# Performance work log

Measured on AMD Instinct MI355X. Metric: run time of the kernel, lower is better.

Reference implementation:

```python
import jax, jax.numpy as jnp
import numpy as np

H = 3072           # hidden_size
I = 8192           # intermediate_size
GS = 128           # quantization group size
B, S = 2, 2048


def dequant(qw, qz, scales, group_size=GS):
    """Group-wise int4 dequant: w = (q - zero) * scale.
    qw: [out, in] int8 nibbles in [0,16); qz: [out, in//g] int8; scales: [out, in//g] f32.
    """
    zp = jnp.repeat(qz.astype(jnp.float32), group_size, axis=1)
    sc = jnp.repeat(scales, group_size, axis=1)
    return (qw.astype(jnp.float32) - zp) * sc


def setup_inputs() -> dict:
    key = jax.random.key(0)
    ks = jax.random.split(key, 8)
    hidden_states = jax.random.normal(ks[0], (B, S, H), dtype=jnp.float32)
    # gate_up projection: [2*I, H], group-quantized along the input (H) dim
    gup_qw = jax.random.randint(ks[1], (2 * I, H), 0, 16, dtype=jnp.int8)
    gup_qz = jax.random.randint(ks[2], (2 * I, H // GS), 0, 16, dtype=jnp.int8)
    gup_scales = jax.random.uniform(ks[3], (2 * I, H // GS), dtype=jnp.float32, minval=0.005, maxval=0.02)
    # down projection: [H, I], group-quantized along the input (I) dim
    down_qw = jax.random.randint(ks[4], (H, I), 0, 16, dtype=jnp.int8)
    down_qz = jax.random.randint(ks[5], (H, I // GS), 0, 16, dtype=jnp.int8)
    down_scales = jax.random.uniform(ks[6], (H, I // GS), dtype=jnp.float32, minval=0.005, maxval=0.02)
    down_bias = jnp.zeros((H,), dtype=jnp.float32)
    return {
        "hidden_states": hidden_states,
        "gup_qw": gup_qw, "gup_qz": gup_qz, "gup_scales": gup_scales,
        "down_qw": down_qw, "down_qz": down_qz, "down_scales": down_scales,
        "down_bias": down_bias,
    }


def reference(hidden_states, gup_qw, gup_qz, gup_scales, down_qw, down_qz, down_scales, down_bias):
    W_gup = dequant(gup_qw, gup_qz, gup_scales)           # [2I, H]
    up_states = jnp.einsum('bsh,oh->bso', hidden_states, W_gup)  # [B,S,2I]
    gate, up = jnp.split(up_states, 2, axis=-1)
    act = jax.nn.silu(gate) * up                          # fused gate*act*up
    W_down = dequant(down_qw, down_qz, down_scales)       # [H, I]
    out = jnp.einsum('bsi,hi->bsh', act, W_down) + down_bias
    return out
```

## Files before the change

kernel.cpp:

```cpp
#include <hip/hip_runtime.h>


typedef float f32x4 __attribute__((ext_vector_type(4)));
typedef float f32x2 __attribute__((ext_vector_type(2)));
typedef int   i32x4 __attribute__((ext_vector_type(4)));

__device__ __forceinline__ void gload16(const void* g, void* l) {
  __builtin_amdgcn_global_load_lds(
      (const __attribute__((address_space(1))) void*)g,
      (__attribute__((address_space(3))) void*)l, 16, 0, 0);
}

__global__ __launch_bounds__(256) void quant_x(const float* __restrict__ x,
                                               signed char* __restrict__ Xq,
                                               float* __restrict__ Xs4) {
  int g    = blockIdx.x;
  int rq   = blockIdx.y;
  int w    = threadIdx.x >> 6;
  int lane = threadIdx.x & 63;
  int row  = rq * 4 + w;
  __shared__ float wmax[4];
  const float2 v = *(const float2*)(x + (size_t)row * 3072 + g * 128 + lane * 2);
  float m = fmaxf(fabsf(v.x), fabsf(v.y));
#pragma unroll
  for (int s = 1; s < 64; s <<= 1) m = fmaxf(m, __shfl_xor(m, s));
  if (lane == 0) wmax[w] = m;
  __syncthreads();
  float m4 = fmaxf(fmaxf(wmax[0], wmax[1]), fmaxf(wmax[2], wmax[3]));
  float inv = m4 > 0.f ? 127.f / m4 : 0.f;
  int qa = (int)rintf(v.x * inv);
  int qb = (int)rintf(v.y * inv);
  unsigned short pk = (unsigned short)((qa & 0xff) | ((qb & 0xff) << 8));
  *(unsigned short*)(Xq + (size_t)row * 3072 + g * 128 + lane * 2) = pk;
  if (threadIdx.x == 0) Xs4[g * 1024 + rq] = m4 * (1.f / 127.f);
}

template <int K>
__global__ __launch_bounds__(256) void requant_k(const int* __restrict__ qw,
                                                 const int* __restrict__ qz,
                                                 signed char* __restrict__ W) {
  constexpr int KG = K / 128;
  constexpr int perrow = K / 8;
  int idx = blockIdx.x * 256 + threadIdx.x;
  int row = idx / perrow;
  int c8  = idx - row * perrow;
  int k   = c8 << 3;
  int z   = qz[row * KG + (k >> 7)];
  const int4* q4 = (const int4*)(qw + (size_t)row * K + k);
  int4 qa = q4[0];
  int4 qb = q4[1];
  int b0 = ((qa.x - z) & 0xff) | (((qa.y - z) & 0xff) << 8) |
           (((qa.z - z) & 0xff) << 16) | (((qa.w - z) & 0xff) << 24);
  int b1 = ((qb.x - z) & 0xff) | (((qb.y - z) & 0xff) << 8) |
           (((qb.z - z) & 0xff) << 16) | (((qb.w - z) & 0xff) << 24);
  int2 o; o.x = b0; o.y = b1;
  *(int2*)(W + (size_t)row * K + k) = o;
}

__global__ __launch_bounds__(256) void transpose_sc(const float* __restrict__ in,
                                                    float* __restrict__ out,
                                                    int R, int G) {
  int idx = blockIdx.x * 256 + threadIdx.x;
  int r = idx / G;
  int g = idx - r * G;
  out[(size_t)g * R + r] = in[idx];
}


__global__ __launch_bounds__(256, 2) void gemm_gateup_i8(
    const signed char* __restrict__ Xq, const signed char* __restrict__ Wq,
    const float* __restrict__ Xs4,
    const float* __restrict__ GsT,
    signed char* __restrict__ act,
    float* __restrict__ As4) {
  const int K = 3072;
  const int bid = blockIdx.x;
  const int xcd = bid & 7;
  const int jb  = bid >> 3;
  const int n0  = ((xcd << 3) + (jb & 7)) * 128;
  const int m0  = (jb >> 3) * 128;
  __shared__ signed char lA[16384];
  __shared__ signed char lG[16384];
  __shared__ signed char lU[16384];
  __shared__ float rmax[2][128];
  __shared__ float rmax4[32];

  const int tid  = threadIdx.x;
  const int l    = tid & 63;
  const int quad = l >> 4;
  const int l16  = l & 15;
  const int wcI  = (tid >> 6) & 1;
  const int wr   = ((tid >> 6) >> 1) * 64;
  const int wc   = wcI * 64;

  f32x2 fg[4][4][2] = {};
  f32x2 fu[4][4][2] = {};

  int off[4];
#pragma unroll
  for (int jj = 0; jj < 4; ++jj) {
    int c   = tid + 256 * jj;
    int row = c >> 3;
    int log = (c & 7) ^ (row & 7);
    off[jj] = row * K + log * 16;
  }
  const signed char* baseA = Xq + (size_t)m0 * K;
  const signed char* baseG = Wq + (size_t)n0 * K;
  const signed char* baseU = Wq + (size_t)(8192 + n0) * K;

  int aoff[2][4], boff[2][4];
#pragma unroll
  for (int h = 0; h < 2; ++h) {
    int slot = h * 4 + quad;
#pragma unroll
    for (int i = 0; i < 4; ++i) {
      int ra = wr + i * 16 + l16;
      aoff[h][i] = ra * 128 + ((slot ^ (ra & 7)) * 16);
      int rb = wc + i * 16 + l16;
      boff[h][i] = rb * 128 + ((slot ^ (rb & 7)) * 16);
    }
  }
  const int qbase = (m0 >> 2) + (wr >> 2) + quad;

  for (int g = 0; g < 24; ++g) {
    const int kk = g << 7;
#pragma unroll
    for (int jj = 0; jj < 4; ++jj) {
      gload16(baseA + off[jj] + kk, lA + (tid + 256 * jj) * 16);
      gload16(baseG + off[jj] + kk, lG + (tid + 256 * jj) * 16);
      gload16(baseU + off[jj] + kk, lU + (tid + 256 * jj) * 16);
    }
    float sxq[4], sg[4], su[4];
#pragma unroll
    for (int i = 0; i < 4; ++i) sxq[i] = Xs4[g * 1024 + qbase + i * 4];
#pragma unroll
    for (int jj = 0; jj < 4; ++jj) {
      sg[jj] = GsT[g * 16384 + n0 + wc + jj * 16 + l16];
      su[jj] = GsT[g * 16384 + 8192 + n0 + wc + jj * 16 + l16];
    }
    __syncthreads();

    i32x4 a[4][2];
#pragma unroll
    for (int i = 0; i < 4; ++i) {
      a[i][0] = *(const i32x4*)(lA + aoff[0][i]);
      a[i][1] = *(const i32x4*)(lA + aoff[1][i]);
    }
#pragma unroll
    for (int jj = 0; jj < 4; ++jj) {
      i32x4 bg0 = *(const i32x4*)(lG + boff[0][jj]);
      i32x4 bg1 = *(const i32x4*)(lG + boff[1][jj]);
      i32x4 bu0 = *(const i32x4*)(lU + boff[0][jj]);
      i32x4 bu1 = *(const i32x4*)(lU + boff[1][jj]);
#pragma unroll
      for (int i = 0; i < 4; ++i) {
        i32x4 zero = {0, 0, 0, 0};
        i32x4 ig = __builtin_amdgcn_mfma_i32_16x16x64_i8(a[i][0], bg0, zero, 0, 0, 0);
        ig = __builtin_amdgcn_mfma_i32_16x16x64_i8(a[i][1], bg1, ig, 0, 0, 0);
        i32x4 iu = __builtin_amdgcn_mfma_i32_16x16x64_i8(a[i][0], bu0, zero, 0, 0, 0);
        iu = __builtin_amdgcn_mfma_i32_16x16x64_i8(a[i][1], bu1, iu, 0, 0, 0);
        float pgs = sxq[i] * sg[jj];
        float pus = sxq[i] * su[jj];
        f32x2 pg2 = {pgs, pgs};
        f32x2 pu2 = {pus, pus};
        f32x2 g01 = {(float)ig[0], (float)ig[1]};
        f32x2 g23 = {(float)ig[2], (float)ig[3]};
        f32x2 u01 = {(float)iu[0], (float)iu[1]};
        f32x2 u23 = {(float)iu[2], (float)iu[3]};
        fg[i][jj][0] = __builtin_elementwise_fma(g01, pg2, fg[i][jj][0]);
        fg[i][jj][1] = __builtin_elementwise_fma(g23, pg2, fg[i][jj][1]);
        fu[i][jj][0] = __builtin_elementwise_fma(u01, pu2, fu[i][jj][0]);
        fu[i][jj][1] = __builtin_elementwise_fma(u23, pu2, fu[i][jj][1]);
      }
    }
    __syncthreads();
  }

  float av[4][4][4];
#pragma unroll
  for (int i = 0; i < 4; ++i)
#pragma unroll
    for (int jj = 0; jj < 4; ++jj)
#pragma unroll
      for (int r = 0; r < 4; ++r) {
        float gv = fg[i][jj][r >> 1][r & 1];
        float uv = fu[i][jj][r >> 1][r & 1];
        av[i][jj][r] = (gv / (1.f + __expf(-gv))) * uv;
      }

#pragma unroll
  for (int i = 0; i < 4; ++i)
#pragma unroll
    for (int r = 0; r < 4; ++r) {
      float m = 0.f;
#pragma unroll
      for (int jj = 0; jj < 4; ++jj) m = fmaxf(m, fabsf(av[i][jj][r]));
      m = fmaxf(m, __shfl_xor(m, 1));
      m = fmaxf(m, __shfl_xor(m, 2));
      m = fmaxf(m, __shfl_xor(m, 4));
      m = fmaxf(m, __shfl_xor(m, 8));
      if (l16 == 0) rmax[wcI][wr + i * 16 + quad * 4 + r] = m;
    }
  __syncthreads();
  if (tid < 32) {
    float m = 0.f;
#pragma unroll
    for (int k = 0; k < 4; ++k)
      m = fmaxf(m, fmaxf(rmax[0][tid * 4 + k], rmax[1][tid * 4 + k]));
    rmax4[tid] = m;
    As4[(n0 >> 7) * 1024 + (m0 >> 2) + tid] = m * (1.f / 127.f);
  }
  __syncthreads();

#pragma unroll
  for (int i = 0; i < 4; ++i) {
    float mx = rmax4[(wr >> 2) + i * 4 + quad];
    float inv = mx > 0.f ? 127.f / mx : 0.f;
#pragma unroll
    for (int r = 0; r < 4; ++r) {
      int mrow = wr + i * 16 + quad * 4 + r;
#pragma unroll
      for (int jj = 0; jj < 4; ++jj) {
        int q = (int)rintf(av[i][jj][r] * inv);
        lA[mrow * 128 + wc + jj * 16 + l16] = (signed char)q;
      }
    }
  }
  __syncthreads();

#pragma unroll
  for (int t = 0; t < 4; ++t) {
    int c = tid + 256 * t;
    int row = c >> 3;
    int col = (c & 7) * 16;
    *(int4*)(act + (size_t)(m0 + row) * 8192 + n0 + col) = *(const int4*)(lA + row * 128 + col);
  }
}

__global__ __launch_bounds__(256, 2) void gemm_down_i8(
    const signed char* __restrict__ Aq, const signed char* __restrict__ Wq,
    const float* __restrict__ As4,
    const float* __restrict__ DsT,
    const float* __restrict__ bias,
    float* __restrict__ out) {
  const int K = 8192;
  const int bid = blockIdx.x;
  const int xcd = bid & 7;
  const int jb  = bid >> 3;
  const int jn  = jb % 12;
  const int jm  = jb / 12;
  const int n0  = (12 * (xcd & 1) + jn) * 128;
  const int m0  = (8 * (xcd >> 1) + jm) * 128;
  __shared__ signed char lA[16384];
  __shared__ signed char lB[16384];

  const int tid  = threadIdx.x;
  const int l    = tid & 63;
  const int quad = l >> 4;
  const int l16  = l & 15;
  const int wr   = ((tid >> 6) >> 1) * 64;
  const int wc   = ((tid >> 6) & 1) * 64;

  f32x2 fc[4][4][2] = {};

  int off[4];
#pragma unroll
  for (int jj = 0; jj < 4; ++jj) {
    int c   = tid + 256 * jj;
    int row = c >> 3;
    int log = (c & 7) ^ (row & 7);
    off[jj] = row * K + log * 16;
  }
  const signed char* baseA = Aq + (size_t)m0 * K;
  const signed char* baseB = Wq + (size_t)n0 * K;

  int aoff[2][4], boff[2][4];
#pragma unroll
  for (int h = 0; h < 2; ++h) {
    int slot = h * 4 + quad;
#pragma unroll
    for (int i = 0; i < 4; ++i) {
      int ra = wr + i * 16 + l16;
      aoff[h][i] = ra * 128 + ((slot ^ (ra & 7)) * 16);
      int rb = wc + i * 16 + l16;
      boff[h][i] = rb * 128 + ((slot ^ (rb & 7)) * 16);
    }
  }
  const int qbase = (m0 >> 2) + (wr >> 2) + quad;

  for (int g = 0; g < 64; ++g) {
    const int kk = g << 7;
#pragma unroll
    for (int jj = 0; jj < 4; ++jj) {
      gload16(baseA + off[jj] + kk, lA + (tid + 256 * jj) * 16);
      gload16(baseB + off[jj] + kk, lB + (tid + 256 * jj) * 16);
    }
    float sxq[4], sn[4];
#pragma unroll
    for (int i = 0; i < 4; ++i) sxq[i] = As4[g * 1024 + qbase + i * 4];
#pragma unroll
    for (int jj = 0; jj < 4; ++jj)
      sn[jj] = DsT[g * 3072 + n0 + wc + jj * 16 + l16];
    __syncthreads();

    i32x4 a[4][2];
#pragma unroll
    for (int i = 0; i < 4; ++i) {
      a[i][0] = *(const i32x4*)(lA + aoff[0][i]);
      a[i][1] = *(const i32x4*)(lA + aoff[1][i]);
    }
#pragma unroll
    for (int jj = 0; jj < 4; ++jj) {
      i32x4 b0 = *(const i32x4*)(lB + boff[0][jj]);
      i32x4 b1 = *(const i32x4*)(lB + boff[1][jj]);
#pragma unroll
      for (int i = 0; i < 4; ++i) {
        i32x4 zero = {0, 0, 0, 0};
        i32x4 ic = __builtin_amdgcn_mfma_i32_16x16x64_i8(a[i][0], b0, zero, 0, 0, 0);
        ic = __builtin_amdgcn_mfma_i32_16x16x64_i8(a[i][1], b1, ic, 0, 0, 0);
        float ps = sxq[i] * sn[jj];
        f32x2 p2 = {ps, ps};
        f32x2 c01 = {(float)ic[0], (float)ic[1]};
        f32x2 c23 = {(float)ic[2], (float)ic[3]};
        fc[i][jj][0] = __builtin_elementwise_fma(c01, p2, fc[i][jj][0]);
        fc[i][jj][1] = __builtin_elementwise_fma(c23, p2, fc[i][jj][1]);
      }
    }
    __syncthreads();
  }

  float bj[4];
#pragma unroll
  for (int jj = 0; jj < 4; ++jj) bj[jj] = bias[n0 + wc + jj * 16 + l16];

#pragma unroll
  for (int i = 0; i < 4; ++i)
#pragma unroll
    for (int jj = 0; jj < 4; ++jj)
#pragma unroll
      for (int r = 0; r < 4; ++r) {
        int m = m0 + wr + i * 16 + quad * 4 + r;
        int n = n0 + wc + jj * 16 + l16;
        out[(size_t)m * 3072 + n] = fc[i][jj][r >> 1][r & 1] + bj[jj];
      }
}

extern "C" void kernel_launch(void* const* d_in, const int* in_sizes, int n_in,
                              void* d_out, int out_size, void* d_ws, size_t ws_size,
                              hipStream_t stream) {
  const float* x        = (const float*)d_in[0];
  const int*   gup_qw   = (const int*)d_in[1];
  const int*   gup_qz   = (const int*)d_in[2];
  const float* gup_sc   = (const float*)d_in[3];
  const int*   down_qw  = (const int*)d_in[4];
  const int*   down_qz  = (const int*)d_in[5];
  const float* down_sc  = (const float*)d_in[6];
  const float* down_b   = (const float*)d_in[7];
  float* out = (float*)d_out;

  char* ws = (char*)d_ws;
  signed char* Xq    = (signed char*)(ws);
  signed char* Wgupq = (signed char*)(ws + 12582912);
  signed char* Wdnq  = (signed char*)(ws + 62914560);
  signed char* Actq  = (signed char*)(ws + 88080384);
  float* Xs4 = (float*)(ws + 121634816);
  float* GsT = (float*)(ws + 121733120);
  float* DsT = (float*)(ws + 123305984);
  float* As4 = (float*)(ws + 124092416);

  quant_x<<<dim3(24, 1024), 256, 0, stream>>>(x, Xq, Xs4);
  requant_k<3072><<<24576, 256, 0, stream>>>(gup_qw, gup_qz, Wgupq);
  requant_k<8192><<<12288, 256, 0, stream>>>(down_qw, down_qz, Wdnq);
  transpose_sc<<<1536, 256, 0, stream>>>(gup_sc, GsT, 16384, 24);
  transpose_sc<<<768, 256, 0, stream>>>(down_sc, DsT, 3072, 64);
  gemm_gateup_i8<<<2048, 256, 0, stream>>>(Xq, Wgupq, Xs4, GsT, Actq, As4);
  gemm_down_i8<<<768, 256, 0, stream>>>(Actq, Wdnq, As4, DsT, down_b, out);
}
```

Measured before the change: 799.0 us.

## Double-buffer LDS tiles in both int8 GEMMs and widen gate-up block to 512 threads

Both GEMMs now prefetch the next K-tile into a second LDS buffer while the MFMAs run on the current one. This replaces the load-then-sync-then-compute pattern with a single waitcnt+barrier per iteration, and wave priority is raised during the MFMA section. The gate-up kernel also moves to 512 threads (8 waves, each covering a 64x32 sub-tile) to cut per-thread accumulators and add waves. The cost is more LDS: 96KB for gate-up, which limits blocks per CU and may reduce occupancy.

```diff
diff --git a/kernel.cpp b/kernel.cpp
--- a/kernel.cpp
+++ b/kernel.cpp
@@ -67,7 +67,7 @@
 }
 
 
-__global__ __launch_bounds__(256, 2) void gemm_gateup_i8(
+__global__ __launch_bounds__(512, 2) void gemm_gateup_i8(
     const signed char* __restrict__ Xq, const signed char* __restrict__ Wq,
     const float* __restrict__ Xs4,
     const float* __restrict__ GsT,
@@ -79,36 +79,34 @@
   const int jb  = bid >> 3;
   const int n0  = ((xcd << 3) + (jb & 7)) * 128;
   const int m0  = (jb >> 3) * 128;
-  __shared__ signed char lA[16384];
-  __shared__ signed char lG[16384];
-  __shared__ signed char lU[16384];
-  __shared__ float rmax[2][128];
+  __shared__ __align__(16) signed char smem[98304];
+  __shared__ float rmax[4][128];
   __shared__ float rmax4[32];
 
   const int tid  = threadIdx.x;
   const int l    = tid & 63;
   const int quad = l >> 4;
   const int l16  = l & 15;
-  const int wcI  = (tid >> 6) & 1;
-  const int wr   = ((tid >> 6) >> 1) * 64;
-  const int wc   = wcI * 64;
-
-  f32x2 fg[4][4][2] = {};
-  f32x2 fu[4][4][2] = {};
-
-  int off[4];
-#pragma unroll
-  for (int jj = 0; jj < 4; ++jj) {
-    int c   = tid + 256 * jj;
+  const int w    = tid >> 6;
+  const int wr   = (w >> 2) * 64;
+  const int wc   = (w & 3) * 32;
+
+  f32x2 fg[4][2][2] = {};
+  f32x2 fu[4][2][2] = {};
+
+  int off[2];
+#pragma unroll
+  for (int t = 0; t < 2; ++t) {
+    int c   = tid + 512 * t;
     int row = c >> 3;
     int log = (c & 7) ^ (row & 7);
-    off[jj] = row * K + log * 16;
+    off[t] = row * K + log * 16;
   }
   const signed char* baseA = Xq + (size_t)m0 * K;
   const signed char* baseG = Wq + (size_t)n0 * K;
   const signed char* baseU = Wq + (size_t)(8192 + n0) * K;
 
-  int aoff[2][4], boff[2][4];
+  int aoff[2][4], boff[2][2];
 #pragma unroll
   for (int h = 0; h < 2; ++h) {
     int slot = h * 4 + quad;
@@ -116,42 +114,66 @@
     for (int i = 0; i < 4; ++i) {
       int ra = wr + i * 16 + l16;
       aoff[h][i] = ra * 128 + ((slot ^ (ra & 7)) * 16);
-      int rb = wc + i * 16 + l16;
-      boff[h][i] = rb * 128 + ((slot ^ (rb & 7)) * 16);
+    }
+#pragma unroll
+    for (int jj = 0; jj < 2; ++jj) {
+      int rb = wc + jj * 16 + l16;
+      boff[h][jj] = rb * 128 + ((slot ^ (rb & 7)) * 16);
     }
   }
   const int qbase = (m0 >> 2) + (wr >> 2) + quad;
 
+#pragma unroll
+  for (int t = 0; t < 2; ++t) {
+    gload16(baseA + off[t], smem + (tid + 512 * t) * 16);
+    gload16(baseG + off[t], smem + 16384 + (tid + 512 * t) * 16);
+    gload16(baseU + off[t], smem + 32768 + (tid + 512 * t) * 16);
+  }
+
+  int cur = 0;
   for (int g = 0; g < 24; ++g) {
-    const int kk = g << 7;
-#pragma unroll
-    for (int jj = 0; jj < 4; ++jj) {
-      gload16(baseA + off[jj] + kk, lA + (tid + 256 * jj) * 16);
-      gload16(baseG + off[jj] + kk, lG + (tid + 256 * jj) * 16);
-      gload16(baseU + off[jj] + kk, lU + (tid + 256 * jj) * 16);
-    }
-    float sxq[4], sg[4], su[4];
+    asm volatile("s_waitcnt vmcnt(0)" ::: "memory");
+    __builtin_amdgcn_s_barrier();
+    __builtin_amdgcn_sched_barrier(0);
+
+    float sxq[4], sg[2], su[2];
 #pragma unroll
     for (int i = 0; i < 4; ++i) sxq[i] = Xs4[g * 1024 + qbase + i * 4];
 #pragma unroll
-    for (int jj = 0; jj < 4; ++jj) {
+    for (int jj = 0; jj < 2; ++jj) {
       sg[jj] = GsT[g * 16384 + n0 + wc + jj * 16 + l16];
       su[jj] = GsT[g * 16384 + 8192 + n0 + wc + jj * 16 + l16];
     }
-    __syncthreads();
+    __builtin_amdgcn_sched_barrier(0);
+
+    if (g < 23) {
+      const int s1 = (cur ^ 1) * 49152;
+      const int kk = (g + 1) << 7;
+#pragma unroll
+      for (int t = 0; t < 2; ++t) {
+        gload16(baseA + off[t] + kk, smem + s1 + (tid + 512 * t) * 16);
+        gload16(baseG + off[t] + kk, smem + s1 + 16384 + (tid + 512 * t) * 16);
+        gload16(baseU + off[t] + kk, smem + s1 + 32768 + (tid + 512 * t) * 16);
+      }
+    }
+
+    const signed char* A0 = smem + cur * 49152;
+    const signed char* G0 = A0 + 16384;
+    const signed char* U0 = A0 + 32768;
 
     i32x4 a[4][2];
 #pragma unroll
     for (int i = 0; i < 4; ++i) {
-      a[i][0] = *(const i32x4*)(lA + aoff[0][i]);
-      a[i][1] = *(const i32x4*)(lA + aoff[1][i]);
-    }
-#pragma unroll
-    for (int jj = 0; jj < 4; ++jj) {
-      i32x4 bg0 = *(const i32x4*)(lG + boff[0][jj]);
-      i32x4 bg1 = *(const i32x4*)(lG + boff[1][jj]);
-      i32x4 bu0 = *(const i32x4*)(lU + boff[0][jj]);
-      i32x4 bu1 = *(const i32x4*)(lU + boff[1][jj]);
+      a[i][0] = *(const i32x4*)(A0 + aoff[0][i]);
+      a[i][1] = *(const i32x4*)(A0 + aoff[1][i]);
+    }
+    __builtin_amdgcn_s_setprio(1);
+#pragma unroll
+    for (int jj = 0; jj < 2; ++jj) {
+      i32x4 bg0 = *(const i32x4*)(G0 + boff[0][jj]);
+      i32x4 bg1 = *(const i32x4*)(G0 + boff[1][jj]);
+      i32x4 bu0 = *(const i32x4*)(U0 + boff[0][jj]);
+      i32x4 bu1 = *(const i32x4*)(U0 + boff[1][jj]);
 #pragma unroll
       for (int i = 0; i < 4; ++i) {
         i32x4 zero = {0, 0, 0, 0};
@@ -173,14 +195,15 @@
         fu[i][jj][1] = __builtin_elementwise_fma(u23, pu2, fu[i][jj][1]);
       }
     }
-    __syncthreads();
-  }
-
-  float av[4][4][4];
+    __builtin_amdgcn_s_setprio(0);
+    cur ^= 1;
+  }
+
+  float av[4][2][4];
 #pragma unroll
   for (int i = 0; i < 4; ++i)
 #pragma unroll
-    for (int jj = 0; jj < 4; ++jj)
+    for (int jj = 0; jj < 2; ++jj)
 #pragma unroll
       for (int r = 0; r < 4; ++r) {
         float gv = fg[i][jj][r >> 1][r & 1];
@@ -192,21 +215,20 @@
   for (int i = 0; i < 4; ++i)
 #pragma unroll
     for (int r = 0; r < 4; ++r) {
-      float m = 0.f;
-#pragma unroll
-      for (int jj = 0; jj < 4; ++jj) m = fmaxf(m, fabsf(av[i][jj][r]));
+      float m = fmaxf(fabsf(av[i][0][r]), fabsf(av[i][1][r]));
       m = fmaxf(m, __shfl_xor(m, 1));
       m = fmaxf(m, __shfl_xor(m, 2));
       m = fmaxf(m, __shfl_xor(m, 4));
       m = fmaxf(m, __shfl_xor(m, 8));
-      if (l16 == 0) rmax[wcI][wr + i * 16 + quad * 4 + r] = m;
+      if (l16 == 0) rmax[w & 3][wr + i * 16 + quad * 4 + r] = m;
     }
   __syncthreads();
   if (tid < 32) {
     float m = 0.f;
 #pragma unroll
-    for (int k = 0; k < 4; ++k)
-      m = fmaxf(m, fmaxf(rmax[0][tid * 4 + k], rmax[1][tid * 4 + k]));
+    for (int c = 0; c < 4; ++c)
+#pragma unroll
+      for (int k = 0; k < 4; ++k) m = fmaxf(m, rmax[c][tid * 4 + k]);
     rmax4[tid] = m;
     As4[(n0 >> 7) * 1024 + (m0 >> 2) + tid] = m * (1.f / 127.f);
   }
@@ -220,20 +242,20 @@
     for (int r = 0; r < 4; ++r) {
       int mrow = wr + i * 16 + quad * 4 + r;
 #pragma unroll
-      for (int jj = 0; jj < 4; ++jj) {
+      for (int jj = 0; jj < 2; ++jj) {
         int q = (int)rintf(av[i][jj][r] * inv);
-        lA[mrow * 128 + wc + jj * 16 + l16] = (signed char)q;
+        smem[mrow * 128 + wc + jj * 16 + l16] = (signed char)q;
       }
     }
   }
   __syncthreads();
 
 #pragma unroll
-  for (int t = 0; t < 4; ++t) {
-    int c = tid + 256 * t;
+  for (int t = 0; t < 2; ++t) {
+    int c = tid + 512 * t;
     int row = c >> 3;
     int col = (c & 7) * 16;
-    *(int4*)(act + (size_t)(m0 + row) * 8192 + n0 + col) = *(const int4*)(lA + row * 128 + col);
+    *(int4*)(act + (size_t)(m0 + row) * 8192 + n0 + col) = *(const int4*)(smem + row * 128 + col);
   }
 }
 
@@ -251,8 +273,7 @@
   const int jm  = jb / 12;
   const int n0  = (12 * (xcd & 1) + jn) * 128;
   const int m0  = (8 * (xcd >> 1) + jm) * 128;
-  __shared__ signed char lA[16384];
-  __shared__ signed char lB[16384];
+  __shared__ __align__(16) signed char smem[65536];
 
   const int tid  = threadIdx.x;
   const int l    = tid & 63;
@@ -288,31 +309,50 @@
   }
   const int qbase = (m0 >> 2) + (wr >> 2) + quad;
 
+#pragma unroll
+  for (int jj = 0; jj < 4; ++jj) {
+    gload16(baseA + off[jj], smem + (tid + 256 * jj) * 16);
+    gload16(baseB + off[jj], smem + 16384 + (tid + 256 * jj) * 16);
+  }
+
+  int cur = 0;
   for (int g = 0; g < 64; ++g) {
-    const int kk = g << 7;
-#pragma unroll
-    for (int jj = 0; jj < 4; ++jj) {
-      gload16(baseA + off[jj] + kk, lA + (tid + 256 * jj) * 16);
-      gload16(baseB + off[jj] + kk, lB + (tid + 256 * jj) * 16);
-    }
+    asm volatile("s_waitcnt vmcnt(0)" ::: "memory");
+    __builtin_amdgcn_s_barrier();
+    __builtin_amdgcn_sched_barrier(0);
+
     float sxq[4], sn[4];
 #pragma unroll
     for (int i = 0; i < 4; ++i) sxq[i] = As4[g * 1024 + qbase + i * 4];
 #pragma unroll
     for (int jj = 0; jj < 4; ++jj)
       sn[jj] = DsT[g * 3072 + n0 + wc + jj * 16 + l16];
-    __syncthreads();
+    __builtin_amdgcn_sched_barrier(0);
+
+    if (g < 63) {
+      const int s1 = (cur ^ 1) * 32768;
+      const int kk = (g + 1) << 7;
+#pragma unroll
+      for (int jj = 0; jj < 4; ++jj) {
+        gload16(baseA + off[jj] + kk, smem + s1 + (tid + 256 * jj) * 16);
+        gload16(baseB + off[jj] + kk, smem + s1 + 16384 + (tid + 256 * jj) * 16);
+      }
+    }
+
+    const signed char* A0 = smem + cur * 32768;
+    const signed char* B0 = A0 + 16384;
 
     i32x4 a[4][2];
 #pragma unroll
     for (int i = 0; i < 4; ++i) {
-      a[i][0] = *(const i32x4*)(lA + aoff[0][i]);
-      a[i][1] = *(const i32x4*)(lA + aoff[1][i]);
-    }
+      a[i][0] = *(const i32x4*)(A0 + aoff[0][i]);
+      a[i][1] = *(const i32x4*)(A0 + aoff[1][i]);
+    }
+    __builtin_amdgcn_s_setprio(1);
 #pragma unroll
     for (int jj = 0; jj < 4; ++jj) {
-      i32x4 b0 = *(const i32x4*)(lB + boff[0][jj]);
-      i32x4 b1 = *(const i32x4*)(lB + boff[1][jj]);
+      i32x4 b0 = *(const i32x4*)(B0 + boff[0][jj]);
+      i32x4 b1 = *(const i32x4*)(B0 + boff[1][jj]);
 #pragma unroll
       for (int i = 0; i < 4; ++i) {
         i32x4 zero = {0, 0, 0, 0};
@@ -326,7 +366,8 @@
         fc[i][jj][1] = __builtin_elementwise_fma(c23, p2, fc[i][jj][1]);
       }
     }
-    __syncthreads();
+    __builtin_amdgcn_s_setprio(0);
+    cur ^= 1;
   }
 
   float bj[4];
@@ -373,6 +414,6 @@
   requant_k<8192><<<12288, 256, 0, stream>>>(down_qw, down_qz, Wdnq);
   transpose_sc<<<1536, 256, 0, stream>>>(gup_sc, GsT, 16384, 24);
   transpose_sc<<<768, 256, 0, stream>>>(down_sc, DsT, 3072, 64);
-  gemm_gateup_i8<<<2048, 256, 0, stream>>>(Xq, Wgupq, Xs4, GsT, Actq, As4);
+  gemm_gateup_i8<<<2048, 512, 0, stream>>>(Xq, Wgupq, Xs4, GsT, Actq, As4);
   gemm_down_i8<<<768, 256, 0, stream>>>(Actq, Wdnq, As4, DsT, down_b, out);
 }
```

New measurement: 958.2 us. 19.9% more time.

## Use per-row scales for gate/up GEMM and accumulate int32 across K

Applied to the files above, without the earlier changes.

Activations are now quantized with one scale per 4-row block across the full hidden dimension instead of per 128-wide group. Gate/up weights are requantized to int8 with a single per-row scale that folds in the group scales, so the GEMM can accumulate in int32 over all of K and apply the scale once in the epilogue. This removes per-group int-to-float conversion and FMA work from the inner loop, along with the gate/up scale transpose kernel. It also adds s_setprio around the MFMA sections of both GEMMs. The trade-off is coarser quantization, which adds more rounding error to the weights and activations.

```diff
diff --git a/kernel.cpp b/kernel.cpp
--- a/kernel.cpp
+++ b/kernel.cpp
@@ -11,28 +11,68 @@
       (__attribute__((address_space(3))) void*)l, 16, 0, 0);
 }
 
-__global__ __launch_bounds__(256) void quant_x(const float* __restrict__ x,
-                                               signed char* __restrict__ Xq,
-                                               float* __restrict__ Xs4) {
-  int g    = blockIdx.x;
-  int rq   = blockIdx.y;
+__global__ __launch_bounds__(256) void quant_x_flat(const float* __restrict__ x,
+                                                    signed char* __restrict__ Xq,
+                                                    float* __restrict__ Xs) {
+  int rq   = blockIdx.x;
   int w    = threadIdx.x >> 6;
   int lane = threadIdx.x & 63;
-  int row  = rq * 4 + w;
+  size_t rowbase = ((size_t)rq * 4 + w) * 3072;
   __shared__ float wmax[4];
-  const float2 v = *(const float2*)(x + (size_t)row * 3072 + g * 128 + lane * 2);
-  float m = fmaxf(fabsf(v.x), fabsf(v.y));
+  float4 v[12];
+  float m = 0.f;
+#pragma unroll
+  for (int it = 0; it < 12; ++it) {
+    v[it] = *(const float4*)(x + rowbase + (lane + it * 64) * 4);
+    m = fmaxf(m, fmaxf(fmaxf(fabsf(v[it].x), fabsf(v[it].y)),
+                       fmaxf(fabsf(v[it].z), fabsf(v[it].w))));
+  }
 #pragma unroll
   for (int s = 1; s < 64; s <<= 1) m = fmaxf(m, __shfl_xor(m, s));
   if (lane == 0) wmax[w] = m;
   __syncthreads();
   float m4 = fmaxf(fmaxf(wmax[0], wmax[1]), fmaxf(wmax[2], wmax[3]));
   float inv = m4 > 0.f ? 127.f / m4 : 0.f;
-  int qa = (int)rintf(v.x * inv);
-  int qb = (int)rintf(v.y * inv);
-  unsigned short pk = (unsigned short)((qa & 0xff) | ((qb & 0xff) << 8));
-  *(unsigned short*)(Xq + (size_t)row * 3072 + g * 128 + lane * 2) = pk;
-  if (threadIdx.x == 0) Xs4[g * 1024 + rq] = m4 * (1.f / 127.f);
+#pragma unroll
+  for (int it = 0; it < 12; ++it) {
+    int a = (int)rintf(v[it].x * inv);
+    int b = (int)rintf(v[it].y * inv);
+    int c = (int)rintf(v[it].z * inv);
+    int d = (int)rintf(v[it].w * inv);
+    int pk = (a & 0xff) | ((b & 0xff) << 8) | ((c & 0xff) << 16) | ((d & 0xff) << 24);
+    *(int*)(Xq + rowbase + (lane + it * 64) * 4) = pk;
+  }
+  if (threadIdx.x == 0) Xs[rq] = m4 * (1.f / 127.f);
+}
+
+__global__ __launch_bounds__(256) void requant_gup_flat(const int* __restrict__ qw,
+                                                        const int* __restrict__ qz,
+                                                        const float* __restrict__ sc,
+                                                        signed char* __restrict__ W,
+                                                        float* __restrict__ Ws) {
+  int w    = threadIdx.x >> 6;
+  int lane = threadIdx.x & 63;
+  int r    = blockIdx.x * 4 + w;
+  float smax = (lane < 24) ? sc[r * 24 + lane] : 0.f;
+#pragma unroll
+  for (int s = 1; s < 64; s <<= 1) smax = fmaxf(smax, __shfl_xor(smax, s));
+  float rs    = smax * (15.f / 127.f);
+  float invrs = 127.f / (15.f * smax);
+#pragma unroll
+  for (int it = 0; it < 12; ++it) {
+    int cidx = lane + it * 64;
+    int g    = cidx >> 5;
+    int z    = qz[r * 24 + g];
+    float f  = sc[r * 24 + g] * invrs;
+    int4 q   = *(const int4*)(qw + (size_t)r * 3072 + cidx * 4);
+    int a = (int)rintf((float)(q.x - z) * f);
+    int b = (int)rintf((float)(q.y - z) * f);
+    int c = (int)rintf((float)(q.z - z) * f);
+    int d = (int)rintf((float)(q.w - z) * f);
+    int pk = (a & 0xff) | ((b & 0xff) << 8) | ((c & 0xff) << 16) | ((d & 0xff) << 24);
+    *(int*)(W + (size_t)r * 3072 + cidx * 4) = pk;
+  }
+  if (lane == 0) Ws[r] = rs;
 }
 
 template <int K>
@@ -69,8 +109,8 @@
 
 __global__ __launch_bounds__(256, 2) void gemm_gateup_i8(
     const signed char* __restrict__ Xq, const signed char* __restrict__ Wq,
-    const float* __restrict__ Xs4,
-    const float* __restrict__ GsT,
+    const float* __restrict__ Xs,
+    const float* __restrict__ WsG,
     signed char* __restrict__ act,
     float* __restrict__ As4) {
   const int K = 3072;
@@ -93,8 +133,8 @@
   const int wr   = ((tid >> 6) >> 1) * 64;
   const int wc   = wcI * 64;
 
-  f32x2 fg[4][4][2] = {};
-  f32x2 fu[4][4][2] = {};
+  i32x4 accg[4][4] = {};
+  i32x4 accu[4][4] = {};
 
   int off[4];
 #pragma unroll
@@ -130,14 +170,6 @@
       gload16(baseG + off[jj] + kk, lG + (tid + 256 * jj) * 16);
       gload16(baseU + off[jj] + kk, lU + (tid + 256 * jj) * 16);
     }
-    float sxq[4], sg[4], su[4];
-#pragma unroll
-    for (int i = 0; i < 4; ++i) sxq[i] = Xs4[g * 1024 + qbase + i * 4];
-#pragma unroll
-    for (int jj = 0; jj < 4; ++jj) {
-      sg[jj] = GsT[g * 16384 + n0 + wc + jj * 16 + l16];
-      su[jj] = GsT[g * 16384 + 8192 + n0 + wc + jj * 16 + l16];
-    }
     __syncthreads();
 
     i32x4 a[4][2];
@@ -146,6 +178,7 @@
       a[i][0] = *(const i32x4*)(lA + aoff[0][i]);
       a[i][1] = *(const i32x4*)(lA + aoff[1][i]);
     }
+    __builtin_amdgcn_s_setprio(1);
 #pragma unroll
     for (int jj = 0; jj < 4; ++jj) {
       i32x4 bg0 = *(const i32x4*)(lG + boff[0][jj]);
@@ -154,39 +187,39 @@
       i32x4 bu1 = *(const i32x4*)(lU + boff[1][jj]);
 #pragma unroll
       for (int i = 0; i < 4; ++i) {
-        i32x4 zero = {0, 0, 0, 0};
-        i32x4 ig = __builtin_amdgcn_mfma_i32_16x16x64_i8(a[i][0], bg0, zero, 0, 0, 0);
-        ig = __builtin_amdgcn_mfma_i32_16x16x64_i8(a[i][1], bg1, ig, 0, 0, 0);
-        i32x4 iu = __builtin_amdgcn_mfma_i32_16x16x64_i8(a[i][0], bu0, zero, 0, 0, 0);
-        iu = __builtin_amdgcn_mfma_i32_16x16x64_i8(a[i][1], bu1, iu, 0, 0, 0);
-        float pgs = sxq[i] * sg[jj];
-        float pus = sxq[i] * su[jj];
-        f32x2 pg2 = {pgs, pgs};
-        f32x2 pu2 = {pus, pus};
-        f32x2 g01 = {(float)ig[0], (float)ig[1]};
-        f32x2 g23 = {(float)ig[2], (float)ig[3]};
-        f32x2 u01 = {(float)iu[0], (float)iu[1]};
-        f32x2 u23 = {(float)iu[2], (float)iu[3]};
-        fg[i][jj][0] = __builtin_elementwise_fma(g01, pg2, fg[i][jj][0]);
-        fg[i][jj][1] = __builtin_elementwise_fma(g23, pg2, fg[i][jj][1]);
-        fu[i][jj][0] = __builtin_elementwise_fma(u01, pu2, fu[i][jj][0]);
-        fu[i][jj][1] = __builtin_elementwise_fma(u23, pu2, fu[i][jj][1]);
+        accg[i][jj] = __builtin_amdgcn_mfma_i32_16x16x64_i8(a[i][0], bg0, accg[i][jj], 0, 0, 0);
+        accg[i][jj] = __builtin_amdgcn_mfma_i32_16x16x64_i8(a[i][1], bg1, accg[i][jj], 0, 0, 0);
+        accu[i][jj] = __builtin_amdgcn_mfma_i32_16x16x64_i8(a[i][0], bu0, accu[i][jj], 0, 0, 0);
+        accu[i][jj] = __builtin_amdgcn_mfma_i32_16x16x64_i8(a[i][1], bu1, accu[i][jj], 0, 0, 0);
       }
     }
+    __builtin_amdgcn_s_setprio(0);
     __syncthreads();
   }
 
+  float sxf[4], wsg[4], wsu[4];
+#pragma unroll
+  for (int i = 0; i < 4; ++i) sxf[i] = Xs[qbase + i * 4];
+#pragma unroll
+  for (int jj = 0; jj < 4; ++jj) {
+    wsg[jj] = WsG[n0 + wc + jj * 16 + l16];
+    wsu[jj] = WsG[8192 + n0 + wc + jj * 16 + l16];
+  }
+
   float av[4][4][4];
 #pragma unroll
   for (int i = 0; i < 4; ++i)
 #pragma unroll
-    for (int jj = 0; jj < 4; ++jj)
+    for (int jj = 0; jj < 4; ++jj) {
+      float pg = sxf[i] * wsg[jj];
+      float pu = sxf[i] * wsu[jj];
 #pragma unroll
       for (int r = 0; r < 4; ++r) {
-        float gv = fg[i][jj][r >> 1][r & 1];
-        float uv = fu[i][jj][r >> 1][r & 1];
+        float gv = (float)accg[i][jj][r] * pg;
+        float uv = (float)accu[i][jj][r] * pu;
         av[i][jj][r] = (gv / (1.f + __expf(-gv))) * uv;
       }
+    }
 
 #pragma unroll
   for (int i = 0; i < 4; ++i)
@@ -309,6 +342,7 @@
       a[i][0] = *(const i32x4*)(lA + aoff[0][i]);
       a[i][1] = *(const i32x4*)(lA + aoff[1][i]);
     }
+    __builtin_amdgcn_s_setprio(1);
 #pragma unroll
     for (int jj = 0; jj < 4; ++jj) {
       i32x4 b0 = *(const i32x4*)(lB + boff[0][jj]);
@@ -326,6 +360,7 @@
         fc[i][jj][1] = __builtin_elementwise_fma(c23, p2, fc[i][jj][1]);
       }
     }
+    __builtin_amdgcn_s_setprio(0);
     __syncthreads();
   }
 
@@ -363,16 +398,15 @@
   signed char* Wgupq = (signed char*)(ws + 12582912);
   signed char* Wdnq  = (signed char*)(ws + 62914560);
   signed char* Actq  = (signed char*)(ws + 88080384);
-  float* Xs4 = (float*)(ws + 121634816);
-  float* GsT = (float*)(ws + 121733120);
-  float* DsT = (float*)(ws + 123305984);
-  float* As4 = (float*)(ws + 124092416);
-
-  quant_x<<<dim3(24, 1024), 256, 0, stream>>>(x, Xq, Xs4);
-  requant_k<3072><<<24576, 256, 0, stream>>>(gup_qw, gup_qz, Wgupq);
+  float* Xs  = (float*)(ws + 121634816);
+  float* WsG = (float*)(ws + 121638912);
+  float* DsT = (float*)(ws + 121704448);
+  float* As4 = (float*)(ws + 122490880);
+
+  quant_x_flat<<<1024, 256, 0, stream>>>(x, Xq, Xs);
+  requant_gup_flat<<<4096, 256, 0, stream>>>(gup_qw, gup_qz, gup_sc, Wgupq, WsG);
   requant_k<8192><<<12288, 256, 0, stream>>>(down_qw, down_qz, Wdnq);
-  transpose_sc<<<1536, 256, 0, stream>>>(gup_sc, GsT, 16384, 24);
   transpose_sc<<<768, 256, 0, stream>>>(down_sc, DsT, 3072, 64);
-  gemm_gateup_i8<<<2048, 256, 0, stream>>>(Xq, Wgupq, Xs4, GsT, Actq, As4);
+  gemm_gateup_i8<<<2048, 256, 0, stream>>>(Xq, Wgupq, Xs, WsG, Actq, As4);
   gemm_down_i8<<<768, 256, 0, stream>>>(Actq, Wdnq, As4, DsT, down_b, out);
 }
```

After: 743.4 us. -7.0%, faster.
